# Optimization experiments

Hardware: AMD Instinct MI355X
Metric: run time of the kernel (lower is better)

## Reference

```python
import jax, jax.numpy as jnp
import numpy as np

H, W, C, UP = 32, 32, 1024, 2  # num_patch=(32,32), embed_dim=1024, upsample_rate=2


def setup_inputs() -> dict:
    key = jax.random.key(0)
    k1, k2 = jax.random.split(key)
    x = jax.random.normal(k1, (32, H * W, C), dtype=jnp.float32)
    # keras Conv2D 1x1 kernel (1,1,Cin,Cout) squeezed to (Cin, Cout); Cin = Cout = C//UP
    w = jax.random.normal(k2, (C // UP, C // UP), dtype=jnp.float32) * 0.02
    return {"x": x, "w": w}


def reference(x, w):
    B, L, Cin = x.shape
    assert L == H * W and Cin == C
    xg = x.reshape(B, H, W, C)
    x0 = xg[..., : C // UP]        # [B,H,W,C/2]
    x1 = xg[..., C // UP:]         # [B,H,W,C/2]
    # Row-wise interleave: output rows alternate x0[i], x1[i] -> [B, 2H, W, C/2]
    xi = jnp.stack([x0, x1], axis=2).reshape(B, 2 * H, W, C // UP)
    # 1x1 conv (no bias) == per-pixel linear projection C/2 -> C/2
    y = jnp.einsum('bhwc,cd->bhwd', xi, w)
    # return_vector=True: tokens [B, 2L, C//2]
    return y.reshape(B, L * UP, C // 2)
```

## Files before the change

kernel.cpp:

```cpp
#include <hip/hip_runtime.h>
#include <hip/hip_bf16.h>
#include <stdint.h>

typedef __attribute__((ext_vector_type(4))) float f32x4;
typedef __attribute__((ext_vector_type(8))) short bf16x8;
typedef __attribute__((ext_vector_type(4))) uint32_t u32x4;

#define KD 512
#define ND 512

__device__ __forceinline__ uint32_t pk_bf16(float lo, float hi) {
  uint32_t ulo = __float_as_uint(lo) + 0x8000u;
  uint32_t uhi = __float_as_uint(hi) + 0x8000u;
  return __builtin_amdgcn_perm(uhi, ulo, 0x07060302u);
}

__global__ void wt_kernel(const float* __restrict__ w, uint16_t* __restrict__ wt) {
  __shared__ float tile[32][33];
  const int bx = blockIdx.x, by = blockIdx.y;
  const int tx = threadIdx.x, ty = threadIdx.y;
#pragma unroll
  for (int i = 0; i < 32; i += 8)
    tile[ty + i][tx] = w[(bx * 32 + ty + i) * ND + by * 32 + tx];
  __syncthreads();
#pragma unroll
  for (int i = 0; i < 32; i += 8) {
    uint32_t u = __float_as_uint(tile[tx][ty + i]);
    uint32_t r = (u + 0x7FFFu + ((u >> 16) & 1u)) >> 16;
    wt[(by * 32 + ty + i) * KD + bx * 32 + tx] = (uint16_t)r;
  }
}

__global__ __launch_bounds__(256) void gemm_kernel(
    const float* __restrict__ x, const uint16_t* __restrict__ wt,
    float* __restrict__ out) {
  __shared__ uint16_t As[2][128 * 32];
  __shared__ uint16_t Ws[2][128 * 32];

  const int tid = threadIdx.x;
  const int lane = tid & 63;
  const int wid = tid >> 6;
  const int wr = wid >> 1, wc = wid & 1;

  const int bid = blockIdx.x;
  const int logical = (bid & 7) * 256 + (bid >> 3);
  const int nt = logical & 3;
  const int mt = logical >> 2;
  const int m0 = mt * 128, n0 = nt * 128;

  const int sr = tid >> 1;
  const int sj0 = (tid & 1) * 2;
  const int aRow = m0 + ((sr & 64) | ((sr & 31) << 1) | ((sr >> 5) & 1));
  const float* aPtr = x + aRow * KD + sj0 * 8;
  const uint16_t* wPtr = wt + (n0 + sr) * KD + sj0 * 8;
  const int swz = (sr >> 1) & 3;
  const int wb0 = sr * 64 + ((sj0 ^ swz) << 4);
  const int wb1 = sr * 64 + (((sj0 + 1) ^ swz) << 4);

  const int fr = lane & 15, fj = lane >> 4;
  int aOff[4], bOff[4];
#pragma unroll
  for (int m = 0; m < 4; ++m) {
    int row = wr * 64 + m * 16 + fr;
    aOff[m] = row * 64 + ((fj ^ ((row >> 1) & 3)) << 4);
    int col = wc * 64 + m * 16 + fr;
    bOff[m] = col * 64 + ((fj ^ ((col >> 1) & 3)) << 4);
  }

  f32x4 acc[4][4];
#pragma unroll
  for (int m = 0; m < 4; ++m)
#pragma unroll
    for (int n = 0; n < 4; ++n) acc[m][n] = (f32x4){0.f, 0.f, 0.f, 0.f};

  f32x4 a0 = *(const f32x4*)(aPtr + 0);
  f32x4 a1 = *(const f32x4*)(aPtr + 4);
  f32x4 a2 = *(const f32x4*)(aPtr + 8);
  f32x4 a3 = *(const f32x4*)(aPtr + 12);
  u32x4 w0 = *(const u32x4*)(wPtr + 0);
  u32x4 w1 = *(const u32x4*)(wPtr + 8);
  aPtr += 32; wPtr += 32;

#pragma unroll 2
  for (int t = 0; t < 16; ++t) {
    uint16_t* Ab = As[t & 1];
    uint16_t* Wb = Ws[t & 1];
    u32x4 pa0 = {pk_bf16(a0.x, a0.y), pk_bf16(a0.z, a0.w),
                 pk_bf16(a1.x, a1.y), pk_bf16(a1.z, a1.w)};
    u32x4 pa1 = {pk_bf16(a2.x, a2.y), pk_bf16(a2.z, a2.w),
                 pk_bf16(a3.x, a3.y), pk_bf16(a3.z, a3.w)};
    *(u32x4*)((char*)Ab + wb0) = pa0;
    *(u32x4*)((char*)Ab + wb1) = pa1;
    *(u32x4*)((char*)Wb + wb0) = w0;
    *(u32x4*)((char*)Wb + wb1) = w1;
    __syncthreads();
    if (t < 15) {
      a0 = *(const f32x4*)(aPtr + 0);
      a1 = *(const f32x4*)(aPtr + 4);
      a2 = *(const f32x4*)(aPtr + 8);
      a3 = *(const f32x4*)(aPtr + 12);
      w0 = *(const u32x4*)(wPtr + 0);
      w1 = *(const u32x4*)(wPtr + 8);
      aPtr += 32; wPtr += 32;
    }
    bf16x8 af[4], wf[4];
#pragma unroll
    for (int m = 0; m < 4; ++m) af[m] = *(bf16x8*)((char*)Ab + aOff[m]);
#pragma unroll
    for (int n = 0; n < 4; ++n) wf[n] = *(bf16x8*)((char*)Wb + bOff[n]);
#pragma unroll
    for (int m = 0; m < 4; ++m)
#pragma unroll
      for (int n = 0; n < 4; ++n)
        acc[m][n] = __builtin_amdgcn_mfma_f32_16x16x32_bf16(wf[n], af[m],
                                                            acc[m][n], 0, 0, 0);
  }

  const int orow = m0 + wr * 64 + fr;
  const int ocol = n0 + wc * 64 + (fj << 2);
#pragma unroll
  for (int m = 0; m < 4; ++m)
#pragma unroll
    for (int n = 0; n < 4; ++n)
      *(f32x4*)(out + (orow + m * 16) * ND + ocol + n * 16) = acc[m][n];
}

extern "C" void kernel_launch(void* const* d_in, const int* in_sizes, int n_in,
                              void* d_out, int out_size, void* d_ws, size_t ws_size,
                              hipStream_t stream) {
  const float* x = (const float*)d_in[0];
  const float* w = (const float*)d_in[1];
  float* out = (float*)d_out;
  uint16_t* wt = (uint16_t*)d_ws;

  wt_kernel<<<dim3(16, 16), dim3(32, 8), 0, stream>>>(w, wt);
  gemm_kernel<<<dim3(2048), dim3(256), 0, stream>>>(x, wt, out);
}
```

Measured before the change: 300.4 us.

## Drop LDS staging and feed 32x32 MFMAs directly from global-loaded registers

Rewrites the GEMM so each wave loads its own A rows (fp32, converted to bf16 in registers) and W rows straight from global memory into MFMA operands, removing shared-memory tiles and block-wide barriers. It switches to 32x32x16 MFMAs on a 64x256 block tile, with each wave owning a 64x64 output, and double-buffers the register prefetch over a fully unrolled K loop. The aim is to cut LDS traffic and synchronisation and to raise occupancy via launch bounds. In exchange, A data is re-read from global/L2 by all four waves of a block with less reuse per load.

```diff
diff --git a/kernel.cpp b/kernel.cpp
--- a/kernel.cpp
+++ b/kernel.cpp
@@ -3,6 +3,7 @@
 #include <stdint.h>
 
 typedef __attribute__((ext_vector_type(4))) float f32x4;
+typedef __attribute__((ext_vector_type(16))) float f32x16;
 typedef __attribute__((ext_vector_type(8))) short bf16x8;
 typedef __attribute__((ext_vector_type(4))) uint32_t u32x4;
 
@@ -13,6 +14,14 @@
   uint32_t ulo = __float_as_uint(lo) + 0x8000u;
   uint32_t uhi = __float_as_uint(hi) + 0x8000u;
   return __builtin_amdgcn_perm(uhi, ulo, 0x07060302u);
+}
+
+__device__ __forceinline__ bf16x8 pack8(f32x4 r0, f32x4 r1) {
+  u32x4 p = {pk_bf16(r0.x, r0.y), pk_bf16(r0.z, r0.w),
+             pk_bf16(r1.x, r1.y), pk_bf16(r1.z, r1.w)};
+  union { u32x4 u; bf16x8 b; } c;
+  c.u = p;
+  return c.b;
 }
 
 __global__ void wt_kernel(const float* __restrict__ w, uint16_t* __restrict__ wt) {
@@ -31,98 +40,90 @@
   }
 }
 
-__global__ __launch_bounds__(256) void gemm_kernel(
+__global__ __launch_bounds__(256, 3) void gemm_kernel(
     const float* __restrict__ x, const uint16_t* __restrict__ wt,
     float* __restrict__ out) {
-  __shared__ uint16_t As[2][128 * 32];
-  __shared__ uint16_t Ws[2][128 * 32];
-
   const int tid = threadIdx.x;
   const int lane = tid & 63;
   const int wid = tid >> 6;
-  const int wr = wid >> 1, wc = wid & 1;
+  const int l31 = lane & 31, hi = lane >> 5;
 
   const int bid = blockIdx.x;
   const int logical = (bid & 7) * 256 + (bid >> 3);
-  const int nt = logical & 3;
-  const int mt = logical >> 2;
-  const int m0 = mt * 128, n0 = nt * 128;
+  const int nh = logical & 1;
+  const int mt = logical >> 1;
+  const int m0 = mt * 64;
+  const int n0 = nh * 256 + wid * 64;
 
-  const int sr = tid >> 1;
-  const int sj0 = (tid & 1) * 2;
-  const int aRow = m0 + ((sr & 64) | ((sr & 31) << 1) | ((sr >> 5) & 1));
-  const float* aPtr = x + aRow * KD + sj0 * 8;
-  const uint16_t* wPtr = wt + (n0 + sr) * KD + sj0 * 8;
-  const int swz = (sr >> 1) & 3;
-  const int wb0 = sr * 64 + ((sj0 ^ swz) << 4);
-  const int wb1 = sr * 64 + (((sj0 + 1) ^ swz) << 4);
+  const char* xb = (const char*)x;
+  const char* wb = (const char*)wt;
 
-  const int fr = lane & 15, fj = lane >> 4;
-  int aOff[4], bOff[4];
+  uint32_t aOff[2], wOff[2];
 #pragma unroll
-  for (int m = 0; m < 4; ++m) {
-    int row = wr * 64 + m * 16 + fr;
-    aOff[m] = row * 64 + ((fj ^ ((row >> 1) & 3)) << 4);
-    int col = wc * 64 + m * 16 + fr;
-    bOff[m] = col * 64 + ((fj ^ ((col >> 1) & 3)) << 4);
+  for (int tm = 0; tm < 2; ++tm)
+    aOff[tm] = (uint32_t)(m0 + l31 * 2 + tm) * (KD * 4) + hi * 32;
+#pragma unroll
+  for (int tn = 0; tn < 2; ++tn)
+    wOff[tn] = (uint32_t)(n0 + tn * 32 + l31) * (KD * 2) + hi * 16;
+
+  f32x16 acc[2][2];
+#pragma unroll
+  for (int tm = 0; tm < 2; ++tm)
+#pragma unroll
+    for (int tn = 0; tn < 2; ++tn)
+#pragma unroll
+      for (int e = 0; e < 16; ++e) acc[tm][tn][e] = 0.f;
+
+  f32x4 raw[2][2][2];
+  bf16x8 wf[2][2];
+#pragma unroll
+  for (int tm = 0; tm < 2; ++tm) {
+    raw[0][tm][0] = *(const f32x4*)(xb + aOff[tm] + 0);
+    raw[0][tm][1] = *(const f32x4*)(xb + aOff[tm] + 16);
+    raw[1][tm][0] = *(const f32x4*)(xb + aOff[tm] + 64);
+    raw[1][tm][1] = *(const f32x4*)(xb + aOff[tm] + 80);
+  }
+#pragma unroll
+  for (int tn = 0; tn < 2; ++tn)
+    wf[0][tn] = *(const bf16x8*)(wb + wOff[tn]);
+
+#pragma unroll
+  for (int ks = 0; ks < 32; ++ks) {
+    const int p = ks & 1;
+    bf16x8 af0 = pack8(raw[p][0][0], raw[p][0][1]);
+    bf16x8 af1 = pack8(raw[p][1][0], raw[p][1][1]);
+    if (ks + 2 < 32) {
+#pragma unroll
+      for (int tm = 0; tm < 2; ++tm) {
+        raw[p][tm][0] = *(const f32x4*)(xb + aOff[tm] + (ks + 2) * 64);
+        raw[p][tm][1] = *(const f32x4*)(xb + aOff[tm] + (ks + 2) * 64 + 16);
+      }
+    }
+    if (ks + 1 < 32) {
+#pragma unroll
+      for (int tn = 0; tn < 2; ++tn)
+        wf[(ks + 1) & 1][tn] =
+            *(const bf16x8*)(wb + wOff[tn] + (ks + 1) * 32);
+    }
+    acc[0][0] = __builtin_amdgcn_mfma_f32_32x32x16_bf16(wf[p][0], af0, acc[0][0], 0, 0, 0);
+    acc[0][1] = __builtin_amdgcn_mfma_f32_32x32x16_bf16(wf[p][1], af0, acc[0][1], 0, 0, 0);
+    acc[1][0] = __builtin_amdgcn_mfma_f32_32x32x16_bf16(wf[p][0], af1, acc[1][0], 0, 0, 0);
+    acc[1][1] = __builtin_amdgcn_mfma_f32_32x32x16_bf16(wf[p][1], af1, acc[1][1], 0, 0, 0);
   }
 
-  f32x4 acc[4][4];
 #pragma unroll
-  for (int m = 0; m < 4; ++m)
+  for (int tm = 0; tm < 2; ++tm) {
+    float* op = out + (size_t)(m0 + tm * 32 + l31) * ND;
 #pragma unroll
-    for (int n = 0; n < 4; ++n) acc[m][n] = (f32x4){0.f, 0.f, 0.f, 0.f};
-
-  f32x4 a0 = *(const f32x4*)(aPtr + 0);
-  f32x4 a1 = *(const f32x4*)(aPtr + 4);
-  f32x4 a2 = *(const f32x4*)(aPtr + 8);
-  f32x4 a3 = *(const f32x4*)(aPtr + 12);
-  u32x4 w0 = *(const u32x4*)(wPtr + 0);
-  u32x4 w1 = *(const u32x4*)(wPtr + 8);
-  aPtr += 32; wPtr += 32;
-
-#pragma unroll 2
-  for (int t = 0; t < 16; ++t) {
-    uint16_t* Ab = As[t & 1];
-    uint16_t* Wb = Ws[t & 1];
-    u32x4 pa0 = {pk_bf16(a0.x, a0.y), pk_bf16(a0.z, a0.w),
-                 pk_bf16(a1.x, a1.y), pk_bf16(a1.z, a1.w)};
-    u32x4 pa1 = {pk_bf16(a2.x, a2.y), pk_bf16(a2.z, a2.w),
-                 pk_bf16(a3.x, a3.y), pk_bf16(a3.z, a3.w)};
-    *(u32x4*)((char*)Ab + wb0) = pa0;
-    *(u32x4*)((char*)Ab + wb1) = pa1;
-    *(u32x4*)((char*)Wb + wb0) = w0;
-    *(u32x4*)((char*)Wb + wb1) = w1;
-    __syncthreads();
-    if (t < 15) {
-      a0 = *(const f32x4*)(aPtr + 0);
-      a1 = *(const f32x4*)(aPtr + 4);
-      a2 = *(const f32x4*)(aPtr + 8);
-      a3 = *(const f32x4*)(aPtr + 12);
-      w0 = *(const u32x4*)(wPtr + 0);
-      w1 = *(const u32x4*)(wPtr + 8);
-      aPtr += 32; wPtr += 32;
+    for (int tn = 0; tn < 2; ++tn) {
+#pragma unroll
+      for (int q = 0; q < 4; ++q) {
+        f32x4 v = {acc[tm][tn][q * 4 + 0], acc[tm][tn][q * 4 + 1],
+                   acc[tm][tn][q * 4 + 2], acc[tm][tn][q * 4 + 3]};
+        *(f32x4*)(op + n0 + tn * 32 + q * 8 + hi * 4) = v;
+      }
     }
-    bf16x8 af[4], wf[4];
-#pragma unroll
-    for (int m = 0; m < 4; ++m) af[m] = *(bf16x8*)((char*)Ab + aOff[m]);
-#pragma unroll
-    for (int n = 0; n < 4; ++n) wf[n] = *(bf16x8*)((char*)Wb + bOff[n]);
-#pragma unroll
-    for (int m = 0; m < 4; ++m)
-#pragma unroll
-      for (int n = 0; n < 4; ++n)
-        acc[m][n] = __builtin_amdgcn_mfma_f32_16x16x32_bf16(wf[n], af[m],
-                                                            acc[m][n], 0, 0, 0);
   }
-
-  const int orow = m0 + wr * 64 + fr;
-  const int ocol = n0 + wc * 64 + (fj << 2);
-#pragma unroll
-  for (int m = 0; m < 4; ++m)
-#pragma unroll
-    for (int n = 0; n < 4; ++n)
-      *(f32x4*)(out + (orow + m * 16) * ND + ocol + n * 16) = acc[m][n];
 }
 
 extern "C" void kernel_launch(void* const* d_in, const int* in_sizes, int n_in,
```

Result: slower. 396.4 us (+31.9%).
